# Kernel optimization log

Hardware: AMD Instinct MI355X
Metric: run time of the kernel (lower is better)

Reference implementation:

```python
import jax, jax.numpy as jnp
import numpy as np

N_HEADS = 16


def setup_inputs() -> dict:
    key = jax.random.key(0)
    ks = jax.random.split(key, 5)
    B, S, D = 2, 2048, 1024
    scale = 1.0 / np.sqrt(D)
    return {
        "x": jax.random.normal(ks[0], (B, S, D), dtype=jnp.float32),
        "w_in": jax.random.normal(ks[1], (3 * D, D), dtype=jnp.float32) * scale,
        "b_in": jax.random.normal(ks[2], (3 * D,), dtype=jnp.float32) * 0.01,
        "w_out": jax.random.normal(ks[3], (D, D), dtype=jnp.float32) * scale,
        "b_out": jax.random.normal(ks[4], (D,), dtype=jnp.float32) * 0.01,
        "mask": 1,
    }


def reference(x, w_in, b_in, w_out, b_out, mask):
    b, s, d = x.shape
    h = N_HEADS
    dh = d // h
    # fused QKV projection (torch Linear: x @ W^T + b)
    qkv = jnp.einsum("bsd,ed->bse", x, w_in) + b_in  # [b, s, 3d]
    q, k, v = jnp.split(qkv, 3, axis=-1)
    # [b, s, d] -> [b, h, s, dh]
    q = q.reshape(b, s, h, dh).transpose(0, 2, 1, 3)
    k = k.reshape(b, s, h, dh).transpose(0, 2, 1, 3)
    v = v.reshape(b, s, h, dh).transpose(0, 2, 1, 3)
    att = jnp.einsum("bhqd,bhkd->bhqk", q, k)
    if mask:
        causal = jnp.triu(jnp.ones((s, s), dtype=bool), k=1)
        att = jnp.where(causal, -jnp.inf, att)
    att = att / jnp.sqrt(jnp.asarray(dh, att.dtype))
    att = jax.nn.softmax(att, axis=-1)
    out = jnp.einsum("bhqk,bhkd->bhqd", att, v)  # [b, h, s, dh]
    out = out.transpose(0, 2, 1, 3).reshape(b, s, d)
    return jnp.einsum("bsd,ed->bse", out, w_out) + b_out
```

## Files before the change

kernel.cpp:

```cpp
#include <hip/hip_runtime.h>
#include <hip/hip_bf16.h>
#include <cmath>

typedef __hip_bfloat16 bf16;
typedef short v8s __attribute__((ext_vector_type(8)));
typedef short v4s __attribute__((ext_vector_type(4)));
typedef float v4f __attribute__((ext_vector_type(4)));
typedef float v16f __attribute__((ext_vector_type(16)));
typedef unsigned v4u __attribute__((ext_vector_type(4)));

#define AS1(p) ((__attribute__((address_space(1))) void*)(p))
#define AS3(p) ((__attribute__((address_space(3))) void*)(p))

__device__ __forceinline__ v4f mfma_bf16(v8s a, v8s b, v4f c) {
    return __builtin_amdgcn_mfma_f32_16x16x32_bf16(a, b, c, 0, 0, 0);
}
__device__ __forceinline__ v16f mfma32(v8s a, v8s b, v16f c) {
    return __builtin_amdgcn_mfma_f32_32x32x16_bf16(a, b, c, 0, 0, 0);
}

__device__ __forceinline__ short bf16_bits(float f) {
    return __builtin_bit_cast(short, __float2bfloat16(f));
}

__device__ __forceinline__ v8s pack4(unsigned a, unsigned b, unsigned c, unsigned d) {
    v4u u = {a, b, c, d};
    return __builtin_bit_cast(v8s, u);
}

__global__ __launch_bounds__(256)
void cvt_all(const float* __restrict__ x, const float* __restrict__ w_in,
             const float* __restrict__ w_out, bf16* __restrict__ xb,
             bf16* __restrict__ wib, bf16* __restrict__ wob)
{
    const int i = blockIdx.x * 256 + threadIdx.x;
    const float* src; bf16* dst; int j;
    if (i < 1048576)      { src = x;     dst = xb;  j = i; }
    else if (i < 1835008) { src = w_in;  dst = wib; j = i - 1048576; }
    else                  { src = w_out; dst = wob; j = i - 1835008; }
    const float4 v = ((const float4*)src)[j];
    v4s p;
    p.x = bf16_bits(v.x); p.y = bf16_bits(v.y);
    p.z = bf16_bits(v.z); p.w = bf16_bits(v.w);
    ((v4s*)dst)[j] = p;
}

template<int NF>
__global__ __launch_bounds__(512, 4)
void gemm_bt(const bf16* __restrict__ A, const bf16* __restrict__ Bt,
             const float* __restrict__ bias, bf16* __restrict__ C,
             float* __restrict__ Cf, bf16* __restrict__ VtOut,
             int N, int K, int lda)
{
    constexpr int BN = NF * 32;
    __shared__ __align__(16) bf16 As[2][128 * 32];
    __shared__ __align__(16) bf16 Bs[2][BN * 32];

    const int t    = threadIdx.x;
    const int lane = t & 63;
    const int w    = t >> 6;
    const int l16  = lane & 15;
    const int quad = lane >> 4;

    const int nwg  = gridDim.x * gridDim.y;
    const int orig = blockIdx.y * gridDim.x + blockIdx.x;
    const int swz  = (orig & 7) * (nwg >> 3) + (orig >> 3);
    const int m0   = (swz / gridDim.x) * 128;
    const int n0   = (swz % gridDim.x) * BN;

    const int wm   = (w & 3) * 32;
    const int wn   = (w >> 2) * (NF * 16);

    const v4f zf = {0.f, 0.f, 0.f, 0.f};
    v4f acc[2][NF];
#pragma unroll
    for (int i = 0; i < 2; ++i)
#pragma unroll
        for (int j = 0; j < NF; ++j) acc[i][j] = zf;

    const int sr = t >> 2;
    const int g  = ((t & 3) ^ ((sr >> 1) & 3)) * 8;
    const bf16* gA = A  + (size_t)(m0 + sr) * lda + g;
    const bf16* gB = Bt + (size_t)(n0 + sr) * K + g;

    auto stage = [&](int kt, int buf) {
        const int k0 = kt * 32;
        __builtin_amdgcn_global_load_lds(AS1(gA + k0), AS3((char*)&As[buf][0] + t * 16), 16, 0, 0);
        if (NF == 4 || t < 256)
            __builtin_amdgcn_global_load_lds(AS1(gB + k0), AS3((char*)&Bs[buf][0] + t * 16), 16, 0, 0);
    };

    stage(0, 0);
    const int KT = K >> 5;
    const int xs = ((l16 >> 1) & 3) * 8;
    for (int kt = 0; kt < KT; ++kt) {
        const int buf = kt & 1;
        __syncthreads();
        if (kt + 1 < KT) stage(kt + 1, buf ^ 1);

        v8s af[2], bfr[NF];
#pragma unroll
        for (int mi = 0; mi < 2; ++mi)
            af[mi] = *(const v8s*)(&As[buf][0] + (wm + mi * 16 + l16) * 32
                                   + ((quad * 8) ^ xs));
#pragma unroll
        for (int ni = 0; ni < NF; ++ni)
            bfr[ni] = *(const v8s*)(&Bs[buf][0] + (wn + ni * 16 + l16) * 32
                                    + ((quad * 8) ^ xs));
#pragma unroll
        for (int mi = 0; mi < 2; ++mi)
#pragma unroll
            for (int ni = 0; ni < NF; ++ni)
                acc[mi][ni] = mfma_bf16(af[mi], bfr[ni], acc[mi][ni]);
    }

    if (VtOut != nullptr && n0 >= 2048) {
        const int bb   = m0 >> 11;
        const int srow = (m0 & 2047) + wm;
#pragma unroll
        for (int ni = 0; ni < NF; ++ni) {
            const int col = n0 + wn + ni * 16 + l16;
            const int hd  = col - 2048;
            const float bv = bias[col];
            bf16* vdst = VtOut + (size_t)(bb * 1024 + hd) * 2048 + srow;
#pragma unroll
            for (int mi = 0; mi < 2; ++mi) {
                v4s p;
#pragma unroll
                for (int r = 0; r < 4; ++r)
                    p[r] = bf16_bits(acc[mi][ni][r] + bv);
                *(v4s*)(vdst + mi * 16 + quad * 4) = p;
            }
        }
    } else {
#pragma unroll
        for (int ni = 0; ni < NF; ++ni) {
            const int col = n0 + wn + ni * 16 + l16;
            const float bv = bias[col];
#pragma unroll
            for (int mi = 0; mi < 2; ++mi) {
#pragma unroll
                for (int r = 0; r < 4; ++r) {
                    const int row = m0 + wm + mi * 16 + quad * 4 + r;
                    const float fv = acc[mi][ni][r] + bv;
                    if (Cf) Cf[(size_t)row * N + col] = fv;
                    else    C [(size_t)row * N + col] = __float2bfloat16(fv);
                }
            }
        }
    }
}

#define M_STATIC 14.0f

__device__ __forceinline__ void softpack(v16f s, int kg0, int qg, bool mask, int hi,
                                         float& lsum, v8s& paE, v8s& paO)
{
    float p[16];
#pragma unroll
    for (int r = 0; r < 16; ++r) {
        float pv = __expf(fmaf(s[r], 0.125f, -M_STATIC));
        if (mask) {
            const int kg = kg0 + (r & 3) + 8 * (r >> 2) + 4 * hi;
            if (kg > qg) pv = 0.f;
        }
        lsum += pv;
        p[r] = pv;
    }
    unsigned P0[4], P1[4];
#pragma unroll
    for (int m = 0; m < 4; ++m) {
        asm("v_cvt_pk_bf16_f32 %0, %1, %2" : "=v"(P0[m]) : "v"(p[4 * m]),     "v"(p[4 * m + 1]));
        asm("v_cvt_pk_bf16_f32 %0, %1, %2" : "=v"(P1[m]) : "v"(p[4 * m + 2]), "v"(p[4 * m + 3]));
    }
    auto sA = __builtin_amdgcn_permlane32_swap(P0[0], P0[1], false, false);
    auto sB = __builtin_amdgcn_permlane32_swap(P1[0], P1[1], false, false);
    auto sC = __builtin_amdgcn_permlane32_swap(P0[2], P0[3], false, false);
    auto sD = __builtin_amdgcn_permlane32_swap(P1[2], P1[3], false, false);
    paE = pack4(sA[0], sB[0], sA[1], sB[1]);
    paO = pack4(sC[0], sD[0], sC[1], sD[1]);
}

__global__ __launch_bounds__(256, 4)
void attn(bf16* __restrict__ qkv, const bf16* __restrict__ Vt)
{
    __shared__ __align__(16) bf16 Ks[2][64 * 64];
    __shared__ __align__(16) bf16 Vs[2][64 * 64];

    const int t    = threadIdx.x;
    const int lane = t & 63;
    const int w    = t >> 6;
    const int wq   = w >> 1;
    const int wk   = w & 1;
    const int l31  = lane & 31;
    const int hi   = lane >> 5;
    const int id   = blockIdx.x;
    const int j    = id >> 3;
    const int bh   = (id & 7) * 4 + (j & 3);
    const int qb   = 31 - (j >> 2);
    const int b = bh >> 4, h = bh & 15;
    const int T = qb + 1;
    const int rowq  = qb * 64 + wq * 32;
    const int qg    = rowq + l31;
    const int ndiag = 2 * qb + wq;

    v8s qf[4];
    {
        const bf16* Qb = qkv + (size_t)(b * 2048 + qg) * 3072 + h * 64 + hi * 8;
#pragma unroll
        for (int c = 0; c < 4; ++c) qf[c] = *(const v8s*)(Qb + c * 16);
    }

    const int sl    = t & 31;
    const int chunk = 2 * ((t >> 6) & 3) + ((t >> 5) & 1);
    const bf16* kbase = qkv + (size_t)(b * 2048 + sl) * 3072 + 1024 + h * 64 + chunk * 8;
    const bf16* vbase = Vt + (size_t)(bh * 64 + sl) * 2048 + chunk * 8;

    auto stage = [&](int tile, int bufi) {
        char* kd = (char*)&Ks[bufi][0] + t * 16;
        char* vd = (char*)&Vs[bufi][0] + t * 16;
        const bf16* ks0 = kbase + (size_t)(tile * 64) * 3072;
        const bf16* vs0 = vbase + tile * 64;
        __builtin_amdgcn_global_load_lds(AS1(ks0),                   AS3(kd),        16, 0, 0);
        __builtin_amdgcn_global_load_lds(AS1(ks0 + (size_t)32*3072), AS3(kd + 4096), 16, 0, 0);
        __builtin_amdgcn_global_load_lds(AS1(vs0),                   AS3(vd),        16, 0, 0);
        __builtin_amdgcn_global_load_lds(AS1(vs0 + (size_t)32*2048), AS3(vd + 4096), 16, 0, 0);
    };

    stage(0, 0);

    v16f o0 = {}, o1 = {};
    float lsum = 0.f;
    const int kfoff = wk * 2048 + lane * 8;
    const int vb0   = wk * 1024 + lane * 8;

    for (int tile = 0; tile < T; ++tile) {
        const int buf = tile & 1;
        __syncthreads();
        if (tile + 1 < T) stage(tile + 1, buf ^ 1);

        const int m_ = 2 * tile + wk;
        if (m_ <= ndiag) {
            const bf16* Kb = &Ks[buf][0];
            const bf16* Vb = &Vs[buf][0];

            v16f s = {};
#pragma unroll
            for (int c = 0; c < 4; ++c)
                s = mfma32(*(const v8s*)(Kb + kfoff + c * 512), qf[c], s);

            v8s paE, paO;
            softpack(s, tile * 64 + 32 * wk, qg, m_ == ndiag, hi, lsum, paE, paO);

            o0 = mfma32(paE, *(const v8s*)(Vb + vb0),            o0);
            o1 = mfma32(paE, *(const v8s*)(Vb + vb0 + 4 * 512),  o1);
            o0 = mfma32(paO, *(const v8s*)(Vb + vb0 + 512),      o0);
            o1 = mfma32(paO, *(const v8s*)(Vb + vb0 + 5 * 512),  o1);
        }
    }

    __syncthreads();
    float* Rp = (float*)&Ks[0][0];
    float* Lp = (float*)&Vs[0][0];
    if (wk) {
        float* R = Rp + wq * 2048 + lane * 32;
#pragma unroll
        for (int j2 = 0; j2 < 4; ++j2) {
            v4f a = { o0[4*j2], o0[4*j2+1], o0[4*j2+2], o0[4*j2+3] };
            ((v4f*)R)[j2 ^ (lane & 7)] = a;
        }
#pragma unroll
        for (int j2 = 0; j2 < 4; ++j2) {
            v4f a = { o1[4*j2], o1[4*j2+1], o1[4*j2+2], o1[4*j2+3] };
            ((v4f*)R)[(4 + j2) ^ (lane & 7)] = a;
        }
        Lp[wq * 64 + lane] = lsum;
    }
    __syncthreads();
    if (!wk) {
        const float* R = Rp + wq * 2048 + lane * 32;
#pragma unroll
        for (int j2 = 0; j2 < 4; ++j2) {
            v4f a = ((const v4f*)R)[j2 ^ (lane & 7)];
#pragma unroll
            for (int e = 0; e < 4; ++e) o0[4*j2 + e] += a[e];
        }
#pragma unroll
        for (int j2 = 0; j2 < 4; ++j2) {
            v4f a = ((const v4f*)R)[(4 + j2) ^ (lane & 7)];
#pragma unroll
            for (int e = 0; e < 4; ++e) o1[4*j2 + e] += a[e];
        }
        lsum += Lp[wq * 64 + lane];
        const float lt = lsum + __shfl_xor(lsum, 32);

        bf16* dst0 = qkv + (size_t)(b * 2048 + rowq) * 3072 + 2048 + h * 64 + l31;
#pragma unroll
        for (int r = 0; r < 16; ++r) {
            const int q = (r & 3) + 8 * (r >> 2) + 4 * hi;
            const float rs  = fmaxf(__shfl(lt, q), 1e-30f);
            const float inv = 1.0f / rs;
            bf16* dst = dst0 + (size_t)q * 3072;
            dst[0]  = __float2bfloat16(o0[r] * inv);
            dst[32] = __float2bfloat16(o1[r] * inv);
        }
    }
}

extern "C" void kernel_launch(void* const* d_in, const int* in_sizes, int n_in,
                              void* d_out, int out_size, void* d_ws, size_t ws_size,
                              hipStream_t stream)
{
    (void)in_sizes; (void)n_in; (void)out_size; (void)ws_size;
    const float* x     = (const float*)d_in[0];
    const float* w_in  = (const float*)d_in[1];
    const float* b_in  = (const float*)d_in[2];
    const float* w_out = (const float*)d_in[3];
    const float* b_out = (const float*)d_in[4];
    float* out = (float*)d_out;

    bf16* ws     = (bf16*)d_ws;
    bf16* xb     = ws;
    bf16* w_inb  = xb     + (size_t)4096 * 1024;
    bf16* w_outb = w_inb  + (size_t)3072 * 1024;
    bf16* qkv    = w_outb + (size_t)1024 * 1024;
    bf16* vt     = (bf16*)d_out;

    cvt_all<<<8192, 256, 0, stream>>>(x, w_in, w_out, xb, w_inb, w_outb);

    gemm_bt<4><<<dim3(24, 32), dim3(512), 0, stream>>>(xb, w_inb, b_in, qkv, nullptr,
                                                       vt, 3072, 1024, 1024);
    attn<<<1024, 256, 0, stream>>>(qkv, vt);
    gemm_bt<2><<<dim3(16, 32), dim3(512), 0, stream>>>(qkv + 2048, w_outb, b_out, nullptr,
                                                       out, nullptr, 1024, 1024, 3072);
}
```

Measured before the change: 187.3 us.

## Give each attention wave its own query rows and drop split-K reduction

The attention kernel now uses 128-row query blocks, with each of the four waves owning 32 query rows and processing both 32-key halves of every K/V tile itself. Before, pairs of waves split each tile along the key axis. This halves the grid, doubles the K/V reuse per staged tile, and removes the end-of-kernel LDS reduction and its extra barriers. In exchange each wave carries more registers (launch bounds lowered to 2), there are fewer blocks to balance the causal workload, and per-wave serial work is longer.

```diff
diff --git a/kernel.cpp b/kernel.cpp
--- a/kernel.cpp
+++ b/kernel.cpp
@@ -181,7 +181,7 @@
     paO = pack4(sC[0], sD[0], sC[1], sD[1]);
 }
 
-__global__ __launch_bounds__(256, 4)
+__global__ __launch_bounds__(256, 2)
 void attn(bf16* __restrict__ qkv, const bf16* __restrict__ Vt)
 {
     __shared__ __align__(16) bf16 Ks[2][64 * 64];
@@ -189,20 +189,18 @@
 
     const int t    = threadIdx.x;
     const int lane = t & 63;
-    const int w    = t >> 6;
-    const int wq   = w >> 1;
-    const int wk   = w & 1;
+    const int wq   = t >> 6;
     const int l31  = lane & 31;
     const int hi   = lane >> 5;
     const int id   = blockIdx.x;
     const int j    = id >> 3;
     const int bh   = (id & 7) * 4 + (j & 3);
-    const int qb   = 31 - (j >> 2);
+    const int qs   = 15 - (j >> 2);
     const int b = bh >> 4, h = bh & 15;
-    const int T = qb + 1;
-    const int rowq  = qb * 64 + wq * 32;
+    const int T = 2 * qs + 2;
+    const int rowq  = qs * 128 + wq * 32;
     const int qg    = rowq + l31;
-    const int ndiag = 2 * qb + wq;
+    const int ndiag = 4 * qs + wq;
 
     v8s qf[4];
     {
@@ -213,97 +211,85 @@
 
     const int sl    = t & 31;
     const int chunk = 2 * ((t >> 6) & 3) + ((t >> 5) & 1);
-    const bf16* kbase = qkv + (size_t)(b * 2048 + sl) * 3072 + 1024 + h * 64 + chunk * 8;
-    const bf16* vbase = Vt + (size_t)(bh * 64 + sl) * 2048 + chunk * 8;
-
-    auto stage = [&](int tile, int bufi) {
+    const bf16* kptr = qkv + (size_t)(b * 2048 + sl) * 3072 + 1024 + h * 64 + chunk * 8;
+    const bf16* vptr = Vt + (size_t)(bh * 64 + sl) * 2048 + chunk * 8;
+
+    auto stage = [&](int bufi) {
         char* kd = (char*)&Ks[bufi][0] + t * 16;
         char* vd = (char*)&Vs[bufi][0] + t * 16;
-        const bf16* ks0 = kbase + (size_t)(tile * 64) * 3072;
-        const bf16* vs0 = vbase + tile * 64;
-        __builtin_amdgcn_global_load_lds(AS1(ks0),                   AS3(kd),        16, 0, 0);
-        __builtin_amdgcn_global_load_lds(AS1(ks0 + (size_t)32*3072), AS3(kd + 4096), 16, 0, 0);
-        __builtin_amdgcn_global_load_lds(AS1(vs0),                   AS3(vd),        16, 0, 0);
-        __builtin_amdgcn_global_load_lds(AS1(vs0 + (size_t)32*2048), AS3(vd + 4096), 16, 0, 0);
+        __builtin_amdgcn_global_load_lds(AS1(kptr),                     AS3(kd),        16, 0, 0);
+        __builtin_amdgcn_global_load_lds(AS1(kptr + (size_t)32 * 3072), AS3(kd + 4096), 16, 0, 0);
+        __builtin_amdgcn_global_load_lds(AS1(vptr),                     AS3(vd),        16, 0, 0);
+        __builtin_amdgcn_global_load_lds(AS1(vptr + (size_t)32 * 2048), AS3(vd + 4096), 16, 0, 0);
     };
 
-    stage(0, 0);
+    stage(0);
+    kptr += (size_t)64 * 3072; vptr += 64;
 
     v16f o0 = {}, o1 = {};
     float lsum = 0.f;
-    const int kfoff = wk * 2048 + lane * 8;
-    const int vb0   = wk * 1024 + lane * 8;
+    const int fb = lane * 8;
 
     for (int tile = 0; tile < T; ++tile) {
         const int buf = tile & 1;
         __syncthreads();
-        if (tile + 1 < T) stage(tile + 1, buf ^ 1);
-
-        const int m_ = 2 * tile + wk;
-        if (m_ <= ndiag) {
-            const bf16* Kb = &Ks[buf][0];
-            const bf16* Vb = &Vs[buf][0];
-
-            v16f s = {};
+        if (tile + 1 < T) {
+            stage(buf ^ 1);
+            kptr += (size_t)64 * 3072; vptr += 64;
+        }
+
+        const int m0_ = 2 * tile;
+        const int m1_ = m0_ + 1;
+        if (m0_ > ndiag) continue;
+
+        const bf16* Kb = &Ks[buf][0];
+        const bf16* Vb = &Vs[buf][0];
+
+        if (m1_ <= ndiag) {
+            v16f s0 = {}, s1 = {};
+#pragma unroll
+            for (int c = 0; c < 4; ++c) {
+                s0 = mfma32(*(const v8s*)(Kb + fb + c * 512),        qf[c], s0);
+                s1 = mfma32(*(const v8s*)(Kb + 2048 + fb + c * 512), qf[c], s1);
+            }
+            v8s paE0, paO0, paE1, paO1;
+            softpack(s0, tile * 64,      qg, false,         hi, lsum, paE0, paO0);
+            softpack(s1, tile * 64 + 32, qg, m1_ == ndiag,  hi, lsum, paE1, paO1);
+
+            o0 = mfma32(paE0, *(const v8s*)(Vb + fb),        o0);
+            o1 = mfma32(paE0, *(const v8s*)(Vb + fb + 2048), o1);
+            o0 = mfma32(paO0, *(const v8s*)(Vb + fb + 512),  o0);
+            o1 = mfma32(paO0, *(const v8s*)(Vb + fb + 2560), o1);
+            o0 = mfma32(paE1, *(const v8s*)(Vb + 1024 + fb),        o0);
+            o1 = mfma32(paE1, *(const v8s*)(Vb + 1024 + fb + 2048), o1);
+            o0 = mfma32(paO1, *(const v8s*)(Vb + 1024 + fb + 512),  o0);
+            o1 = mfma32(paO1, *(const v8s*)(Vb + 1024 + fb + 2560), o1);
+        } else {
+            v16f s0 = {};
 #pragma unroll
             for (int c = 0; c < 4; ++c)
-                s = mfma32(*(const v8s*)(Kb + kfoff + c * 512), qf[c], s);
-
-            v8s paE, paO;
-            softpack(s, tile * 64 + 32 * wk, qg, m_ == ndiag, hi, lsum, paE, paO);
-
-            o0 = mfma32(paE, *(const v8s*)(Vb + vb0),            o0);
-            o1 = mfma32(paE, *(const v8s*)(Vb + vb0 + 4 * 512),  o1);
-            o0 = mfma32(paO, *(const v8s*)(Vb + vb0 + 512),      o0);
-            o1 = mfma32(paO, *(const v8s*)(Vb + vb0 + 5 * 512),  o1);
-        }
-    }
-
-    __syncthreads();
-    float* Rp = (float*)&Ks[0][0];
-    float* Lp = (float*)&Vs[0][0];
-    if (wk) {
-        float* R = Rp + wq * 2048 + lane * 32;
-#pragma unroll
-        for (int j2 = 0; j2 < 4; ++j2) {
-            v4f a = { o0[4*j2], o0[4*j2+1], o0[4*j2+2], o0[4*j2+3] };
-            ((v4f*)R)[j2 ^ (lane & 7)] = a;
-        }
-#pragma unroll
-        for (int j2 = 0; j2 < 4; ++j2) {
-            v4f a = { o1[4*j2], o1[4*j2+1], o1[4*j2+2], o1[4*j2+3] };
-            ((v4f*)R)[(4 + j2) ^ (lane & 7)] = a;
-        }
-        Lp[wq * 64 + lane] = lsum;
-    }
-    __syncthreads();
-    if (!wk) {
-        const float* R = Rp + wq * 2048 + lane * 32;
-#pragma unroll
-        for (int j2 = 0; j2 < 4; ++j2) {
-            v4f a = ((const v4f*)R)[j2 ^ (lane & 7)];
-#pragma unroll
-            for (int e = 0; e < 4; ++e) o0[4*j2 + e] += a[e];
-        }
-#pragma unroll
-        for (int j2 = 0; j2 < 4; ++j2) {
-            v4f a = ((const v4f*)R)[(4 + j2) ^ (lane & 7)];
-#pragma unroll
-            for (int e = 0; e < 4; ++e) o1[4*j2 + e] += a[e];
-        }
-        lsum += Lp[wq * 64 + lane];
-        const float lt = lsum + __shfl_xor(lsum, 32);
-
-        bf16* dst0 = qkv + (size_t)(b * 2048 + rowq) * 3072 + 2048 + h * 64 + l31;
-#pragma unroll
-        for (int r = 0; r < 16; ++r) {
-            const int q = (r & 3) + 8 * (r >> 2) + 4 * hi;
-            const float rs  = fmaxf(__shfl(lt, q), 1e-30f);
-            const float inv = 1.0f / rs;
-            bf16* dst = dst0 + (size_t)q * 3072;
-            dst[0]  = __float2bfloat16(o0[r] * inv);
-            dst[32] = __float2bfloat16(o1[r] * inv);
-        }
+                s0 = mfma32(*(const v8s*)(Kb + fb + c * 512), qf[c], s0);
+            v8s paE0, paO0;
+            softpack(s0, tile * 64, qg, m0_ == ndiag, hi, lsum, paE0, paO0);
+
+            o0 = mfma32(paE0, *(const v8s*)(Vb + fb),        o0);
+            o1 = mfma32(paE0, *(const v8s*)(Vb + fb + 2048), o1);
+            o0 = mfma32(paO0, *(const v8s*)(Vb + fb + 512),  o0);
+            o1 = mfma32(paO0, *(const v8s*)(Vb + fb + 2560), o1);
+        }
+    }
+
+    const float lt = lsum + __shfl_xor(lsum, 32);
+
+    bf16* dst0 = qkv + (size_t)(b * 2048 + rowq) * 3072 + 2048 + h * 64 + l31;
+#pragma unroll
+    for (int r = 0; r < 16; ++r) {
+        const int q = (r & 3) + 8 * (r >> 2) + 4 * hi;
+        const float rs  = fmaxf(__shfl(lt, q), 1e-30f);
+        const float inv = 1.0f / rs;
+        bf16* dst = dst0 + (size_t)q * 3072;
+        dst[0]  = __float2bfloat16(o0[r] * inv);
+        dst[32] = __float2bfloat16(o1[r] * inv);
     }
 }
 
@@ -330,7 +316,7 @@
 
     gemm_bt<4><<<dim3(24, 32), dim3(512), 0, stream>>>(xb, w_inb, b_in, qkv, nullptr,
                                                        vt, 3072, 1024, 1024);
-    attn<<<1024, 256, 0, stream>>>(qkv, vt);
+    attn<<<512, 256, 0, stream>>>(qkv, vt);
     gemm_bt<2><<<dim3(16, 32), dim3(512), 0, stream>>>(qkv + 2048, w_outb, b_out, nullptr,
                                                        out, nullptr, 1024, 1024, 3072);
 }
```

Result: slower. 192.8 us (+3.0%).
